# Performance work log

Hardware: AMD Instinct MI355X
Metric: run time of the kernel (lower is better)

Reference implementation:

```python
import jax, jax.numpy as jnp
import numpy as np

NS, NV = 48, 10            # scalar / vector multiplicities
IN_SIZE = NS + 3*NV + 3*NV + NS   # 156
N_EDGE_FEAT = 96
HIDDEN = 96
# weight shapes per output irrep: 0e:(58,48) 1o:(68,10) 1e:(68,10) 0o:(58,48)
W_SHAPES = [('0e', NS + NV, NS), ('1o', NS + 2*NV, NV), ('1e', 2*NV + NS, NV), ('0o', NV + NS, NS)]
WEIGHT_NUMEL = sum(a*b for _, a, b in W_SHAPES)  # 6928
N_NODES, N_EDGES = 10000, 50000


def setup_inputs() -> dict:
    key = jax.random.key(0)
    ks = jax.random.split(key, 9)
    node_attr = jax.random.normal(ks[0], (N_NODES, IN_SIZE), dtype=jnp.float32)
    edge_index = jax.random.randint(ks[1], (2, N_EDGES), 0, N_NODES)
    edge_attr = jax.random.normal(ks[2], (N_EDGES, N_EDGE_FEAT), dtype=jnp.float32)
    edge_sh = jax.random.normal(ks[3], (N_EDGES, 4), dtype=jnp.float32)
    s1 = 1.0 / np.sqrt(N_EDGE_FEAT)
    s2 = 1.0 / np.sqrt(HIDDEN)
    W1 = jax.random.normal(ks[4], (N_EDGE_FEAT, HIDDEN), dtype=jnp.float32) * s1
    b1 = jnp.zeros((HIDDEN,), dtype=jnp.float32)
    W2 = jax.random.normal(ks[5], (HIDDEN, WEIGHT_NUMEL), dtype=jnp.float32) * s2
    b2 = jnp.zeros((WEIGHT_NUMEL,), dtype=jnp.float32)
    return {'node_attr': node_attr, 'edge_index': edge_index, 'edge_attr': edge_attr,
            'edge_sh': edge_sh, 'W1': W1, 'b1': b1, 'W2': W2, 'b2': b2}


def _faster_tp(in_, sh, weight):
    # in_: [E, 156], sh: [E, 4], weight: [E, 6928]
    in_0e = in_[:, :NS]                                   # [E,48]
    in_1o = in_[:, NS:NS + 3*NV].reshape(-1, NV, 3)       # [E,10,3]
    in_1e = in_[:, NS + 3*NV:NS + 6*NV].reshape(-1, NV, 3)
    in_0o = in_[:, NS + 6*NV:]                            # [E,48]
    sh_0e = sh[:, 0]                                      # [E]
    sh_1o = sh[:, 1:]                                     # [E,3]
    inv_s3 = 1.0 / np.sqrt(3.0)
    inv_s2 = 1.0 / np.sqrt(2.0)

    out_0e = jnp.concatenate([
        in_0e * sh_0e[:, None],
        jnp.sum(in_1o * sh_1o[:, None, :], axis=-1) * inv_s3], axis=-1)      # [E,58]
    out_1o = jnp.concatenate([
        in_0e[:, :, None] * sh_1o[:, None, :],
        in_1o * sh_0e[:, None, None],
        jnp.cross(in_1e, sh_1o[:, None, :]) * inv_s2], axis=-2)              # [E,68,3]
    out_1e = jnp.concatenate([
        jnp.cross(in_1o, sh_1o[:, None, :]) * inv_s2,
        in_1e * sh_0e[:, None, None],
        in_0o[:, :, None] * sh_1o[:, None, :]], axis=-2)                     # [E,68,3]
    out_0o = jnp.concatenate([
        jnp.sum(in_1e * sh_1o[:, None, :], axis=-1) * inv_s3,
        in_0o * sh_0e[:, None]], axis=-1)                                    # [E,58]

    wd = {}
    start = 0
    for name, a, b in W_SHAPES:
        wd[name] = weight[:, start:start + a*b].reshape(-1, a, b) / np.sqrt(a)
        start += a*b

    o0e = jnp.einsum('ei,eio->eo', out_0e, wd['0e'])                 # [E,48]
    o1o = jnp.einsum('eic,eio->eoc', out_1o, wd['1o']).reshape(-1, 3*NV)
    o1e = jnp.einsum('eic,eio->eoc', out_1e, wd['1e']).reshape(-1, 3*NV)
    o0o = jnp.einsum('ei,eio->eo', out_0o, wd['0o'])                 # [E,48]
    return jnp.concatenate([o0e, o1o, o1e, o0o], axis=-1)           # [E,156]


def reference(node_attr, edge_index, edge_attr, edge_sh, W1, b1, W2, b2):
    edge_src, edge_dst = edge_index[0], edge_index[1]
    # edge MLP -> per-edge TP weights
    h = jax.nn.relu(edge_attr @ W1 + b1)
    w = h @ W2 + b2                                       # [E, 6928]
    tp = _faster_tp(node_attr[edge_dst], edge_sh, w)      # [E, 156]
    # scatter-mean over source nodes
    n = node_attr.shape[0]
    seg = jax.ops.segment_sum(tp, edge_src, num_segments=n)
    cnt = jax.ops.segment_sum(jnp.ones((tp.shape[0],), tp.dtype), edge_src, num_segments=n)
    out = seg / jnp.maximum(cnt, 1.0)[:, None]
    # residual (in/out sizes equal, so pad is a no-op)
    return out + node_attr
```

## Files before the change

### kernel.cpp

```cpp
#include <hip/hip_runtime.h>

#define NE 50000
#define NN 10000
#define KH 96
#define WN 6928
#define NTILE 484
#define IN_SZ 156
#define EPW 32

typedef __attribute__((ext_vector_type(8))) short short8;
typedef __attribute__((ext_vector_type(4))) float float4v;

template<int N> struct IC { static constexpr int n = N; };

__device__ __forceinline__ unsigned short f2bf(float x) {
  unsigned u = __float_as_uint(x);
  unsigned r = (u + 0x7FFFu + ((u >> 16) & 1u)) >> 16;
  return (unsigned short)r;
}
__device__ __forceinline__ float b2f(unsigned short u) {
  return __uint_as_float(((unsigned)u) << 16);
}

__device__ __forceinline__ void issue3(short8 (&B)[3], float &bv,
                                       const unsigned short* p, const float* pb) {
  asm volatile("global_load_dwordx4 %0, %4, off\n\t"
               "global_load_dwordx4 %1, %4, off offset:1024\n\t"
               "global_load_dwordx4 %2, %4, off offset:2048\n\t"
               "global_load_dword %3, %5, off"
               : "=&v"(B[0]), "=&v"(B[1]), "=&v"(B[2]), "=&v"(bv)
               : "v"(p), "v"(pb));
}
__device__ __forceinline__ void waitB8(short8 (&B)[3], float &bv) {
  asm volatile("s_waitcnt vmcnt(8)"
               : "+v"(B[0]), "+v"(B[1]), "+v"(B[2]), "+v"(bv));
}
__device__ __forceinline__ void waitB4(short8 (&B)[3], float &bv) {
  asm volatile("s_waitcnt vmcnt(4)"
               : "+v"(B[0]), "+v"(B[1]), "+v"(B[2]), "+v"(bv));
}
__device__ __forceinline__ void waitB0(short8 (&B)[3], float &bv) {
  asm volatile("s_waitcnt vmcnt(0)"
               : "+v"(B[0]), "+v"(B[1]), "+v"(B[2]), "+v"(bv));
}

__device__ __forceinline__ int col_of_np(int np) {
  if (np < 2784) return np;
  if (np < 3872) { int rel = np - 2784, i = rel >> 4, o = rel & 15; return (o < 10) ? 2784 + i * 10 + o : -1; }
  if (np < 4960) { int rel = np - 3872, i = rel >> 4, o = rel & 15; return (o < 10) ? 3464 + i * 10 + o : -1; }
  return 4144 + (np - 4960);
}

#define R0 (NTILE * 192)
#define R1 (R0 + NTILE * 16)
#define R2 (R1 + KH * KH)
#define R3 (R2 + NN * IN_SZ / 4)
#define R4 (R3 + NN / 4)
#define R5 (R4 + 192)
__global__ __launch_bounds__(256) void prep_kernel(
    const float* __restrict__ W2, const float* __restrict__ b2,
    const float* __restrict__ W1,
    unsigned short* __restrict__ W2PT, float* __restrict__ b2PT,
    unsigned short* __restrict__ W1T,
    float* __restrict__ acc, int* __restrict__ icnt,
    unsigned short* __restrict__ h_ext)
{
  int gid = blockIdx.x * 256 + threadIdx.x;
  if (gid < R0) {
    int lane = gid & 63, s = (gid >> 6) % 3, t = gid / 192;
    int l = lane & 15, q = lane >> 4;
    int c = col_of_np(t * 16 + l);
    int kbase = s * 32 + q * 8;
    unsigned short o8[8];
    #pragma unroll
    for (int j = 0; j < 8; ++j) {
      int k = kbase + j;
      float v = (c >= 0) ? W2[(size_t)k * WN + c] : 0.f;
      o8[j] = f2bf(v);
    }
    uint4 pk;
    pk.x = o8[0] | ((unsigned)o8[1] << 16);
    pk.y = o8[2] | ((unsigned)o8[3] << 16);
    pk.z = o8[4] | ((unsigned)o8[5] << 16);
    pk.w = o8[6] | ((unsigned)o8[7] << 16);
    *(uint4*)(W2PT + (size_t)gid * 8) = pk;
  } else if (gid < R1) {
    int j = gid - R0;
    int c = col_of_np(j);
    b2PT[j] = (c >= 0) ? b2[c] : 0.f;
  } else if (gid < R2) {
    int j = gid - R1;
    int c = j / KH, k = j - c * KH;
    W1T[c * KH + k] = f2bf(W1[k * KH + c]);
  } else if (gid < R3) {
    uint4 z = {0, 0, 0, 0};
    ((uint4*)acc)[gid - R2] = z;
  } else if (gid < R4) {
    uint4 z = {0, 0, 0, 0};
    ((uint4*)icnt)[gid - R3] = z;
  } else if (gid < R5) {
    uint4 z = {0, 0, 0, 0};
    ((uint4*)(h_ext + (size_t)NE * KH))[gid - R4] = z;
  }
}

__global__ __launch_bounds__(384) void mlp1_kernel(
    const float* __restrict__ edge_attr, const unsigned short* __restrict__ W1T,
    const float* __restrict__ b1, unsigned short* __restrict__ h_ext)
{
  const int tid = threadIdx.x;
  const int e0 = blockIdx.x * 16;
  const int w = tid >> 6, l = tid & 15, q = (tid >> 4) & 3;

  short8 a[3], b[3];
  #pragma unroll
  for (int s = 0; s < 3; ++s) {
    const float* pa = edge_attr + (size_t)(e0 + l) * KH + s * 32 + q * 8;
    float4 x = *(const float4*)pa, y = *(const float4*)(pa + 4);
    short8 t;
    t[0] = (short)f2bf(x.x); t[1] = (short)f2bf(x.y);
    t[2] = (short)f2bf(x.z); t[3] = (short)f2bf(x.w);
    t[4] = (short)f2bf(y.x); t[5] = (short)f2bf(y.y);
    t[6] = (short)f2bf(y.z); t[7] = (short)f2bf(y.w);
    a[s] = t;
    b[s] = *(const short8*)(W1T + (size_t)(w * 16 + l) * KH + s * 32 + q * 8);
  }
  float4v C = {0.f, 0.f, 0.f, 0.f};
  #pragma unroll
  for (int s = 0; s < 3; ++s)
    C = __builtin_amdgcn_mfma_f32_16x16x32_bf16(a[s], b[s], C, 0, 0, 0);

  float bv = b1[w * 16 + l];
  #pragma unroll
  for (int r = 0; r < 4; ++r)
    h_ext[(size_t)(e0 + q * 4 + r) * KH + w * 16 + l] = f2bf(fmaxf(C[r] + bv, 0.f));
}

__global__ __launch_bounds__(512, 4) void tp_kernel(
    const unsigned short* __restrict__ h_ext, const float* __restrict__ node_attr,
    const int* __restrict__ edge_index, const float* __restrict__ edge_sh,
    const unsigned short* __restrict__ W2PT, const float* __restrict__ b2PT,
    float* __restrict__ acc, int* __restrict__ icnt)
{
  __shared__ float sOut[EPW][IN_SZ];
  __shared__ unsigned short sF0[2][58][EPW];
  __shared__ unsigned short sF1[2][68][3][EPW];
  __shared__ float sShs[EPW][4];
  __shared__ int sSrc[EPW], sDst[EPW];

  const int tid = threadIdx.x;
  const int e0 = blockIdx.x * EPW;

  if (tid < EPW) {
    int ok = (e0 + tid) < NE;
    int s = ok ? edge_index[e0 + tid] : 0;
    int d = ok ? edge_index[NE + e0 + tid] : 0;
    sSrc[tid] = s; sDst[tid] = d;
    if (ok) atomicAdd(&icnt[s], 1);
  }
  if (tid >= 128 && tid < 256) {
    int t2 = tid - 128;
    int e = t2 >> 2, c = t2 & 3;
    sShs[e][c] = ((e0 + e) < NE) ? edge_sh[(size_t)(e0 + e) * 4 + c] : 0.f;
  }
  __syncthreads();

  {
    const int e = tid >> 4, j = tid & 15;
    const float* na = node_attr + (size_t)sDst[e] * IN_SZ;
    const float sh0 = sShs[e][0], sx = sShs[e][1], sy = sShs[e][2], sz = sShs[e][3];
    const float i3 = 0.57735026918962576f, i2 = 0.70710678118654752f;
    for (int i = j; i < 48; i += 16) {
      float v0 = na[i], w0 = na[108 + i];
      sF0[0][i][e] = f2bf(v0 * sh0);
      sF0[1][10 + i][e] = f2bf(w0 * sh0);
      sF1[0][i][0][e] = f2bf(v0 * sx); sF1[0][i][1][e] = f2bf(v0 * sy); sF1[0][i][2][e] = f2bf(v0 * sz);
      sF1[1][20 + i][0][e] = f2bf(w0 * sx); sF1[1][20 + i][1][e] = f2bf(w0 * sy); sF1[1][20 + i][2][e] = f2bf(w0 * sz);
    }
    if (j < 10) {
      const int v = j;
      float ax = na[48 + 3 * v], ay = na[48 + 3 * v + 1], az = na[48 + 3 * v + 2];
      float bx = na[78 + 3 * v], by = na[78 + 3 * v + 1], bz = na[78 + 3 * v + 2];
      sF0[0][48 + v][e] = f2bf((ax * sx + ay * sy + az * sz) * i3);
      sF0[1][v][e]      = f2bf((bx * sx + by * sy + bz * sz) * i3);
      sF1[0][48 + v][0][e] = f2bf(ax * sh0); sF1[0][48 + v][1][e] = f2bf(ay * sh0); sF1[0][48 + v][2][e] = f2bf(az * sh0);
      sF1[0][58 + v][0][e] = f2bf((by * sz - bz * sy) * i2);
      sF1[0][58 + v][1][e] = f2bf((bz * sx - bx * sz) * i2);
      sF1[0][58 + v][2][e] = f2bf((bx * sy - by * sx) * i2);
      sF1[1][v][0][e] = f2bf((ay * sz - az * sy) * i2);
      sF1[1][v][1][e] = f2bf((az * sx - ax * sz) * i2);
      sF1[1][v][2][e] = f2bf((ax * sy - ay * sx) * i2);
      sF1[1][10 + v][0][e] = f2bf(bx * sh0); sF1[1][10 + v][1][e] = f2bf(by * sh0); sF1[1][10 + v][2][e] = f2bf(bz * sh0);
    }
  }
  for (int idx = tid; idx < EPW * IN_SZ; idx += 512) (&sOut[0][0])[idx] = 0.f;
  __syncthreads();

  const int wv = tid >> 6, l = tid & 15, q = (tid >> 4) & 3;

  short8 Af[2][3];
  #pragma unroll
  for (int m = 0; m < 2; ++m) {
    const unsigned short* ar = h_ext + (size_t)(e0 + m * 16 + l) * KH + q * 8;
    #pragma unroll
    for (int s = 0; s < 3; ++s) Af[m][s] = *(const short8*)(ar + s * 32);
  }

  const unsigned short* wlane = W2PT + (size_t)(tid & 63) * 8;
  const float* blane = b2PT + l;

  auto sbody = [&](float (&a0)[4], float (&a1)[4], const short8 (&B)[3], float bv,
                   int sf, int i) {
    ushort4 f0 = *(const ushort4*)&sF0[sf][i][q * 4];
    ushort4 f1 = *(const ushort4*)&sF0[sf][i][16 + q * 4];
    float4v C0 = {bv, bv, bv, bv}, C1 = {bv, bv, bv, bv};
    #pragma unroll
    for (int s2 = 0; s2 < 3; ++s2) {
      C0 = __builtin_amdgcn_mfma_f32_16x16x32_bf16(Af[0][s2], B[s2], C0, 0, 0, 0);
      C1 = __builtin_amdgcn_mfma_f32_16x16x32_bf16(Af[1][s2], B[s2], C1, 0, 0, 0);
    }
    a0[0] += C0[0] * b2f(f0.x); a0[1] += C0[1] * b2f(f0.y);
    a0[2] += C0[2] * b2f(f0.z); a0[3] += C0[3] * b2f(f0.w);
    a1[0] += C1[0] * b2f(f1.x); a1[1] += C1[1] * b2f(f1.y);
    a1[2] += C1[2] * b2f(f1.z); a1[3] += C1[3] * b2f(f1.w);
  };
  auto sflush = [&](float (&a0)[4], float (&a1)[4], int col) {
    #pragma unroll
    for (int r = 0; r < 4; ++r) {
      unsafeAtomicAdd(&sOut[q * 4 + r][col],      a0[r]);
      unsafeAtomicAdd(&sOut[16 + q * 4 + r][col], a1[r]);
    }
  };

  auto run_scalar3 = [&](int sf, int ibeg, int tb, int obase, auto cnt) {
    constexpr int NSTEP = decltype(cnt)::n;
    #pragma unroll 1
    for (int ob = 0; ob < 3; ++ob) {
      float a0[4] = {0.f, 0.f, 0.f, 0.f}, a1[4] = {0.f, 0.f, 0.f, 0.f};
      short8 Ba[3], Bb[3], Bc[3];
      float vA, vB, vC;
      auto tadr = [&](int ii) -> size_t { return (size_t)(tb + 3 * (ibeg + ii) + ob); };
      { size_t t = tadr(0); issue3(Ba, vA, wlane + t * 1536, blane + t * 16); }
      { size_t t = tadr(1); issue3(Bb, vB, wlane + t * 1536, blane + t * 16); }
      { size_t t = tadr(2); issue3(Bc, vC, wlane + t * 1536, blane + t * 16); }
      #pragma unroll 1
      for (int ii = 0; ii < NSTEP - 3; ii += 3) {
        waitB8(Ba, vA); sbody(a0, a1, Ba, vA, sf, ibeg + ii);
        { size_t t = tadr(ii + 3); issue3(Ba, vA, wlane + t * 1536, blane + t * 16); }
        waitB8(Bb, vB); sbody(a0, a1, Bb, vB, sf, ibeg + ii + 1);
        { size_t t = tadr(ii + 4); issue3(Bb, vB, wlane + t * 1536, blane + t * 16); }
        waitB8(Bc, vC); sbody(a0, a1, Bc, vC, sf, ibeg + ii + 2);
        { size_t t = tadr(ii + 5); issue3(Bc, vC, wlane + t * 1536, blane + t * 16); }
      }
      waitB8(Ba, vA); sbody(a0, a1, Ba, vA, sf, ibeg + NSTEP - 3);
      waitB4(Bb, vB); sbody(a0, a1, Bb, vB, sf, ibeg + NSTEP - 2);
      waitB0(Bc, vC); sbody(a0, a1, Bc, vC, sf, ibeg + NSTEP - 1);
      sflush(a0, a1, obase + ob * 16 + l);
    }
  };

  auto run_scalar2 = [&](int sf, int ibeg, int tb, int obase, auto cnt) {
    constexpr int NSTEP = decltype(cnt)::n;
    #pragma unroll 1
    for (int ob = 0; ob < 3; ++ob) {
      float a0[4] = {0.f, 0.f, 0.f, 0.f}, a1[4] = {0.f, 0.f, 0.f, 0.f};
      short8 Ba[3], Bb[3];
      float vA, vB;
      auto tadr = [&](int ii) -> size_t { return (size_t)(tb + 3 * (ibeg + ii) + ob); };
      { size_t t = tadr(0); issue3(Ba, vA, wlane + t * 1536, blane + t * 16); }
      { size_t t = tadr(1); issue3(Bb, vB, wlane + t * 1536, blane + t * 16); }
      #pragma unroll 1
      for (int ii = 0; ii < NSTEP - 2; ii += 2) {
        waitB4(Ba, vA); sbody(a0, a1, Ba, vA, sf, ibeg + ii);
        { size_t t = tadr(ii + 2); issue3(Ba, vA, wlane + t * 1536, blane + t * 16); }
        waitB4(Bb, vB); sbody(a0, a1, Bb, vB, sf, ibeg + ii + 1);
        { size_t t = tadr(ii + 3); issue3(Bb, vB, wlane + t * 1536, blane + t * 16); }
      }
      waitB4(Ba, vA); sbody(a0, a1, Ba, vA, sf, ibeg + NSTEP - 2);
      waitB0(Bb, vB); sbody(a0, a1, Bb, vB, sf, ibeg + NSTEP - 1);
      sflush(a0, a1, obase + ob * 16 + l);
    }
  };

  if (wv < 4) {
    const int sf = wv >> 1;
    run_scalar3(sf, (wv & 1) * 21, sf ? 310 : 0, sf ? 108 : 0, IC<21>{});
  } else {
    const int vf = (wv >> 1) - 2;
    const int ibeg = (wv & 1) * 34;
    const int tb = vf ? 242 : 174;
    float r0[4][3] = {{0.f}}, r1[4][3] = {{0.f}};
    short8 Ba[3], Bb[3];
    float vA, vB;
    auto tadr = [&](int ii) -> size_t { return (size_t)(tb + ibeg + ii); };
    auto vbody = [&](const short8 (&B)[3], float bv, int ii) {
      int i = ibeg + ii;
      ushort4 g0[3], g1[3];
      #pragma unroll
      for (int cc = 0; cc < 3; ++cc) {
        g0[cc] = *(const ushort4*)&sF1[vf][i][cc][q * 4];
        g1[cc] = *(const ushort4*)&sF1[vf][i][cc][16 + q * 4];
      }
      float4v C0 = {bv, bv, bv, bv}, C1 = {bv, bv, bv, bv};
      #pragma unroll
      for (int s = 0; s < 3; ++s) {
        C0 = __builtin_amdgcn_mfma_f32_16x16x32_bf16(Af[0][s], B[s], C0, 0, 0, 0);
        C1 = __builtin_amdgcn_mfma_f32_16x16x32_bf16(Af[1][s], B[s], C1, 0, 0, 0);
      }
      #pragma unroll
      for (int cc = 0; cc < 3; ++cc) {
        r0[0][cc] += C0[0] * b2f(g0[cc].x); r0[1][cc] += C0[1] * b2f(g0[cc].y);
        r0[2][cc] += C0[2] * b2f(g0[cc].z); r0[3][cc] += C0[3] * b2f(g0[cc].w);
        r1[0][cc] += C1[0] * b2f(g1[cc].x); r1[1][cc] += C1[1] * b2f(g1[cc].y);
        r1[2][cc] += C1[2] * b2f(g1[cc].z); r1[3][cc] += C1[3] * b2f(g1[cc].w);
      }
    };
    { size_t t = tadr(0); issue3(Ba, vA, wlane + t * 1536, blane + t * 16); }
    { size_t t = tadr(1); issue3(Bb, vB, wlane + t * 1536, blane + t * 16); }
    #pragma unroll 1
    for (int ii = 0; ii < 32; ii += 2) {
      waitB4(Ba, vA); vbody(Ba, vA, ii);
      { size_t t = tadr(ii + 2); issue3(Ba, vA, wlane + t * 1536, blane + t * 16); }
      waitB4(Bb, vB); vbody(Bb, vB, ii + 1);
      { size_t t = tadr(ii + 3); issue3(Bb, vB, wlane + t * 1536, blane + t * 16); }
    }
    waitB4(Ba, vA); vbody(Ba, vA, 32);
    waitB0(Bb, vB); vbody(Bb, vB, 33);
    if (l < 10) {
      const int col = (vf ? 78 : 48) + 3 * l;
      #pragma unroll
      for (int r = 0; r < 4; ++r)
        #pragma unroll
        for (int cc = 0; cc < 3; ++cc) {
          unsafeAtomicAdd(&sOut[q * 4 + r][col + cc], r0[r][cc]);
          unsafeAtomicAdd(&sOut[16 + q * 4 + r][col + cc], r1[r][cc]);
        }
    }
    run_scalar2(vf, 42 + (wv & 1) * 8, vf ? 310 : 0, vf ? 108 : 0, IC<8>{});
  }
  __syncthreads();

  const float n58 = 0.13130643285972254f, n68 = 0.12126781251816650f;
  for (int idx = tid; idx < EPW * IN_SZ; idx += 512) {
    int e = idx / IN_SZ, o = idx - e * IN_SZ;
    if (e0 + e < NE) {
      float nrm = (o < 48 || o >= 108) ? n58 : n68;
      unsafeAtomicAdd(&acc[(size_t)sSrc[e] * IN_SZ + o], sOut[e][o] * nrm);
    }
  }
}

__global__ __launch_bounds__(256) void finalize_kernel(
    const float* __restrict__ acc, const int* __restrict__ icnt,
    const float* __restrict__ node_attr, float* __restrict__ out)
{
  int idx = blockIdx.x * 256 + threadIdx.x;
  if (idx < NN * IN_SZ) {
    int n = idx / IN_SZ;
    out[idx] = acc[idx] / fmaxf((float)icnt[n], 1.f) + node_attr[idx];
  }
}

extern "C" void kernel_launch(void* const* d_in, const int* in_sizes, int n_in,
                              void* d_out, int out_size, void* d_ws, size_t ws_size,
                              hipStream_t stream)
{
  const float* node_attr  = (const float*)d_in[0];
  const int*   edge_index = (const int*)d_in[1];
  const float* edge_attr  = (const float*)d_in[2];
  const float* edge_sh    = (const float*)d_in[3];
  const float* W1 = (const float*)d_in[4];
  const float* b1 = (const float*)d_in[5];
  const float* W2 = (const float*)d_in[6];
  const float* b2 = (const float*)d_in[7];
  float* out = (float*)d_out;

  unsigned short* h_ext = (unsigned short*)d_ws;
  unsigned short* W2PT  = h_ext + (size_t)50016 * KH;
  float* b2PT = (float*)(W2PT + (size_t)NTILE * 1536);
  float* acc  = b2PT + (size_t)NTILE * 16;
  int*   icnt = (int*)(acc + (size_t)NN * IN_SZ);
  unsigned short* W1T = (unsigned short*)(icnt + NN);

  prep_kernel<<<(R5 + 255) / 256, 256, 0, stream>>>(W2, b2, W1, W2PT, b2PT, W1T,
                                                    acc, icnt, h_ext);
  mlp1_kernel<<<NE / 16, 384, 0, stream>>>(edge_attr, W1T, b1, h_ext);
  tp_kernel<<<(NE + EPW - 1) / EPW, 512, 0, stream>>>(h_ext, node_attr, edge_index,
                                                      edge_sh, W2PT, b2PT, acc, icnt);
  finalize_kernel<<<(NN * IN_SZ + 255) / 256, 256, 0, stream>>>(acc, icnt, node_attr, out);
}
```

Before: 329.0 us.

## Process 64 edges per block to reuse streamed W2 tiles, rebalance wave work

Doubles the edges handled per tp_kernel block from 32 to 64. Each streamed W2 tile now feeds four 16-row MFMA groups instead of two, which roughly halves global W2 traffic per edge. The scalar-path split is reworked so that four waves each cover 30 padded input rows, with zeroed pad rows. Vector waves no longer take a scalar tail. Gathered node attributes are staged once into shared memory as bf16, which adds rounding on the inputs. The trade-offs are higher register and LDS use, launch bounds lowered to 2 blocks per CU, and some imbalance between the scalar and vector waves.

New measurement: 351.3 us. +6.8%, slower.

```diff
diff --git a/kernel.cpp b/kernel.cpp
--- a/kernel.cpp
+++ b/kernel.cpp
@@ -6,12 +6,10 @@
 #define WN 6928
 #define NTILE 484
 #define IN_SZ 156
-#define EPW 32
+#define EPW 64
 
 typedef __attribute__((ext_vector_type(8))) short short8;
 typedef __attribute__((ext_vector_type(4))) float float4v;
-
-template<int N> struct IC { static constexpr int n = N; };
 
 __device__ __forceinline__ unsigned short f2bf(float x) {
   unsigned u = __float_as_uint(x);
@@ -56,7 +54,7 @@
 #define R2 (R1 + KH * KH)
 #define R3 (R2 + NN * IN_SZ / 4)
 #define R4 (R3 + NN / 4)
-#define R5 (R4 + 192)
+#define R5 (R4 + 576)
 __global__ __launch_bounds__(256) void prep_kernel(
     const float* __restrict__ W2, const float* __restrict__ b2,
     const float* __restrict__ W1,
@@ -136,14 +134,15 @@
     h_ext[(size_t)(e0 + q * 4 + r) * KH + w * 16 + l] = f2bf(fmaxf(C[r] + bv, 0.f));
 }
 
-__global__ __launch_bounds__(512, 4) void tp_kernel(
+__global__ __launch_bounds__(512, 2) void tp_kernel(
     const unsigned short* __restrict__ h_ext, const float* __restrict__ node_attr,
     const int* __restrict__ edge_index, const float* __restrict__ edge_sh,
     const unsigned short* __restrict__ W2PT, const float* __restrict__ b2PT,
     float* __restrict__ acc, int* __restrict__ icnt)
 {
+  __shared__ unsigned short sIn[EPW][160];
   __shared__ float sOut[EPW][IN_SZ];
-  __shared__ unsigned short sF0[2][58][EPW];
+  __shared__ unsigned short sF0[2][60][EPW];
   __shared__ unsigned short sF1[2][68][3][EPW];
   __shared__ float sShs[EPW][4];
   __shared__ int sSrc[EPW], sDst[EPW];
@@ -158,29 +157,34 @@
     sSrc[tid] = s; sDst[tid] = d;
     if (ok) atomicAdd(&icnt[s], 1);
   }
-  if (tid >= 128 && tid < 256) {
+  if (tid >= 128 && tid < 384) {
     int t2 = tid - 128;
     int e = t2 >> 2, c = t2 & 3;
     sShs[e][c] = ((e0 + e) < NE) ? edge_sh[(size_t)(e0 + e) * 4 + c] : 0.f;
   }
   __syncthreads();
 
+  for (int idx = tid; idx < EPW * IN_SZ; idx += 512) {
+    int e = idx / IN_SZ, f = idx - e * IN_SZ;
+    sIn[e][f] = f2bf(node_attr[(size_t)sDst[e] * IN_SZ + f]);
+  }
+  for (int idx = tid; idx < EPW * IN_SZ; idx += 512) (&sOut[0][0])[idx] = 0.f;
+  __syncthreads();
+
   {
-    const int e = tid >> 4, j = tid & 15;
-    const float* na = node_attr + (size_t)sDst[e] * IN_SZ;
+    const int e = tid >> 3, j = tid & 7;
     const float sh0 = sShs[e][0], sx = sShs[e][1], sy = sShs[e][2], sz = sShs[e][3];
     const float i3 = 0.57735026918962576f, i2 = 0.70710678118654752f;
-    for (int i = j; i < 48; i += 16) {
-      float v0 = na[i], w0 = na[108 + i];
+    for (int i = j; i < 48; i += 8) {
+      float v0 = b2f(sIn[e][i]), w0 = b2f(sIn[e][108 + i]);
       sF0[0][i][e] = f2bf(v0 * sh0);
       sF0[1][10 + i][e] = f2bf(w0 * sh0);
       sF1[0][i][0][e] = f2bf(v0 * sx); sF1[0][i][1][e] = f2bf(v0 * sy); sF1[0][i][2][e] = f2bf(v0 * sz);
       sF1[1][20 + i][0][e] = f2bf(w0 * sx); sF1[1][20 + i][1][e] = f2bf(w0 * sy); sF1[1][20 + i][2][e] = f2bf(w0 * sz);
     }
-    if (j < 10) {
-      const int v = j;
-      float ax = na[48 + 3 * v], ay = na[48 + 3 * v + 1], az = na[48 + 3 * v + 2];
-      float bx = na[78 + 3 * v], by = na[78 + 3 * v + 1], bz = na[78 + 3 * v + 2];
+    for (int v = j; v < 10; v += 8) {
+      float ax = b2f(sIn[e][48 + 3 * v]), ay = b2f(sIn[e][48 + 3 * v + 1]), az = b2f(sIn[e][48 + 3 * v + 2]);
+      float bx = b2f(sIn[e][78 + 3 * v]), by = b2f(sIn[e][78 + 3 * v + 1]), bz = b2f(sIn[e][78 + 3 * v + 2]);
       sF0[0][48 + v][e] = f2bf((ax * sx + ay * sy + az * sz) * i3);
       sF0[1][v][e]      = f2bf((bx * sx + by * sy + bz * sz) * i3);
       sF1[0][48 + v][0][e] = f2bf(ax * sh0); sF1[0][48 + v][1][e] = f2bf(ay * sh0); sF1[0][48 + v][2][e] = f2bf(az * sh0);
@@ -193,14 +197,17 @@
       sF1[1][10 + v][0][e] = f2bf(bx * sh0); sF1[1][10 + v][1][e] = f2bf(by * sh0); sF1[1][10 + v][2][e] = f2bf(bz * sh0);
     }
   }
-  for (int idx = tid; idx < EPW * IN_SZ; idx += 512) (&sOut[0][0])[idx] = 0.f;
+  if (tid < 256) {
+    int fam = tid >> 7, i = 58 + ((tid >> 6) & 1), e = tid & 63;
+    sF0[fam][i][e] = 0;
+  }
   __syncthreads();
 
   const int wv = tid >> 6, l = tid & 15, q = (tid >> 4) & 3;
 
-  short8 Af[2][3];
+  short8 Af[4][3];
   #pragma unroll
-  for (int m = 0; m < 2; ++m) {
+  for (int m = 0; m < 4; ++m) {
     const unsigned short* ar = h_ext + (size_t)(e0 + m * 16 + l) * KH + q * 8;
     #pragma unroll
     for (int s = 0; s < 3; ++s) Af[m][s] = *(const short8*)(ar + s * 32);
@@ -209,103 +216,93 @@
   const unsigned short* wlane = W2PT + (size_t)(tid & 63) * 8;
   const float* blane = b2PT + l;
 
-  auto sbody = [&](float (&a0)[4], float (&a1)[4], const short8 (&B)[3], float bv,
+  auto sbody = [&](float (&a)[4][4], const short8 (&B)[3], float bv,
                    int sf, int i) {
     ushort4 f0 = *(const ushort4*)&sF0[sf][i][q * 4];
     ushort4 f1 = *(const ushort4*)&sF0[sf][i][16 + q * 4];
-    float4v C0 = {bv, bv, bv, bv}, C1 = {bv, bv, bv, bv};
+    ushort4 f2 = *(const ushort4*)&sF0[sf][i][32 + q * 4];
+    ushort4 f3 = *(const ushort4*)&sF0[sf][i][48 + q * 4];
+    float4v C0 = {bv, bv, bv, bv}, C1 = C0, C2 = C0, C3 = C0;
     #pragma unroll
     for (int s2 = 0; s2 < 3; ++s2) {
       C0 = __builtin_amdgcn_mfma_f32_16x16x32_bf16(Af[0][s2], B[s2], C0, 0, 0, 0);
       C1 = __builtin_amdgcn_mfma_f32_16x16x32_bf16(Af[1][s2], B[s2], C1, 0, 0, 0);
-    }
-    a0[0] += C0[0] * b2f(f0.x); a0[1] += C0[1] * b2f(f0.y);
-    a0[2] += C0[2] * b2f(f0.z); a0[3] += C0[3] * b2f(f0.w);
-    a1[0] += C1[0] * b2f(f1.x); a1[1] += C1[1] * b2f(f1.y);
-    a1[2] += C1[2] * b2f(f1.z); a1[3] += C1[3] * b2f(f1.w);
+      C2 = __builtin_amdgcn_mfma_f32_16x16x32_bf16(Af[2][s2], B[s2], C2, 0, 0, 0);
+      C3 = __builtin_amdgcn_mfma_f32_16x16x32_bf16(Af[3][s2], B[s2], C3, 0, 0, 0);
+    }
+    a[0][0] += C0[0] * b2f(f0.x); a[0][1] += C0[1] * b2f(f0.y);
+    a[0][2] += C0[2] * b2f(f0.z); a[0][3] += C0[3] * b2f(f0.w);
+    a[1][0] += C1[0] * b2f(f1.x); a[1][1] += C1[1] * b2f(f1.y);
+    a[1][2] += C1[2] * b2f(f1.z); a[1][3] += C1[3] * b2f(f1.w);
+    a[2][0] += C2[0] * b2f(f2.x); a[2][1] += C2[1] * b2f(f2.y);
+    a[2][2] += C2[2] * b2f(f2.z); a[2][3] += C2[3] * b2f(f2.w);
+    a[3][0] += C3[0] * b2f(f3.x); a[3][1] += C3[1] * b2f(f3.y);
+    a[3][2] += C3[2] * b2f(f3.z); a[3][3] += C3[3] * b2f(f3.w);
   };
-  auto sflush = [&](float (&a0)[4], float (&a1)[4], int col) {
+  auto sflush = [&](float (&a)[4][4], int col) {
     #pragma unroll
-    for (int r = 0; r < 4; ++r) {
-      unsafeAtomicAdd(&sOut[q * 4 + r][col],      a0[r]);
-      unsafeAtomicAdd(&sOut[16 + q * 4 + r][col], a1[r]);
-    }
+    for (int h = 0; h < 4; ++h)
+      #pragma unroll
+      for (int r = 0; r < 4; ++r)
+        unsafeAtomicAdd(&sOut[h * 16 + q * 4 + r][col], a[h][r]);
   };
 
-  auto run_scalar3 = [&](int sf, int ibeg, int tb, int obase, auto cnt) {
-    constexpr int NSTEP = decltype(cnt)::n;
+  if (wv < 4) {
+    const int sf = wv >> 1;
+    const int ibeg = (wv & 1) * 30;
+    const int tb = sf ? 310 : 0;
+    const int obase = sf ? 108 : 0;
     #pragma unroll 1
     for (int ob = 0; ob < 3; ++ob) {
-      float a0[4] = {0.f, 0.f, 0.f, 0.f}, a1[4] = {0.f, 0.f, 0.f, 0.f};
+      float a[4][4] = {{0.f,0.f,0.f,0.f},{0.f,0.f,0.f,0.f},{0.f,0.f,0.f,0.f},{0.f,0.f,0.f,0.f}};
       short8 Ba[3], Bb[3], Bc[3];
       float vA, vB, vC;
-      auto tadr = [&](int ii) -> size_t { return (size_t)(tb + 3 * (ibeg + ii) + ob); };
+      auto tadr = [&](int ii) -> size_t {
+        int i = ibeg + ii; if (i >= 58) i = ibeg;
+        return (size_t)(tb + 3 * i + ob);
+      };
       { size_t t = tadr(0); issue3(Ba, vA, wlane + t * 1536, blane + t * 16); }
       { size_t t = tadr(1); issue3(Bb, vB, wlane + t * 1536, blane + t * 16); }
       { size_t t = tadr(2); issue3(Bc, vC, wlane + t * 1536, blane + t * 16); }
       #pragma unroll 1
-      for (int ii = 0; ii < NSTEP - 3; ii += 3) {
-        waitB8(Ba, vA); sbody(a0, a1, Ba, vA, sf, ibeg + ii);
+      for (int ii = 0; ii < 27; ii += 3) {
+        waitB8(Ba, vA); sbody(a, Ba, vA, sf, ibeg + ii);
         { size_t t = tadr(ii + 3); issue3(Ba, vA, wlane + t * 1536, blane + t * 16); }
-        waitB8(Bb, vB); sbody(a0, a1, Bb, vB, sf, ibeg + ii + 1);
+        waitB8(Bb, vB); sbody(a, Bb, vB, sf, ibeg + ii + 1);
         { size_t t = tadr(ii + 4); issue3(Bb, vB, wlane + t * 1536, blane + t * 16); }
-        waitB8(Bc, vC); sbody(a0, a1, Bc, vC, sf, ibeg + ii + 2);
+        waitB8(Bc, vC); sbody(a, Bc, vC, sf, ibeg + ii + 2);
         { size_t t = tadr(ii + 5); issue3(Bc, vC, wlane + t * 1536, blane + t * 16); }
       }
-      waitB8(Ba, vA); sbody(a0, a1, Ba, vA, sf, ibeg + NSTEP - 3);
-      waitB4(Bb, vB); sbody(a0, a1, Bb, vB, sf, ibeg + NSTEP - 2);
-      waitB0(Bc, vC); sbody(a0, a1, Bc, vC, sf, ibeg + NSTEP - 1);
-      sflush(a0, a1, obase + ob * 16 + l);
-    }
-  };
-
-  auto run_scalar2 = [&](int sf, int ibeg, int tb, int obase, auto cnt) {
-    constexpr int NSTEP = decltype(cnt)::n;
-    #pragma unroll 1
-    for (int ob = 0; ob < 3; ++ob) {
-      float a0[4] = {0.f, 0.f, 0.f, 0.f}, a1[4] = {0.f, 0.f, 0.f, 0.f};
-      short8 Ba[3], Bb[3];
-      float vA, vB;
-      auto tadr = [&](int ii) -> size_t { return (size_t)(tb + 3 * (ibeg + ii) + ob); };
-      { size_t t = tadr(0); issue3(Ba, vA, wlane + t * 1536, blane + t * 16); }
-      { size_t t = tadr(1); issue3(Bb, vB, wlane + t * 1536, blane + t * 16); }
-      #pragma unroll 1
-      for (int ii = 0; ii < NSTEP - 2; ii += 2) {
-        waitB4(Ba, vA); sbody(a0, a1, Ba, vA, sf, ibeg + ii);
-        { size_t t = tadr(ii + 2); issue3(Ba, vA, wlane + t * 1536, blane + t * 16); }
-        waitB4(Bb, vB); sbody(a0, a1, Bb, vB, sf, ibeg + ii + 1);
-        { size_t t = tadr(ii + 3); issue3(Bb, vB, wlane + t * 1536, blane + t * 16); }
-      }
-      waitB4(Ba, vA); sbody(a0, a1, Ba, vA, sf, ibeg + NSTEP - 2);
-      waitB0(Bb, vB); sbody(a0, a1, Bb, vB, sf, ibeg + NSTEP - 1);
-      sflush(a0, a1, obase + ob * 16 + l);
-    }
-  };
-
-  if (wv < 4) {
-    const int sf = wv >> 1;
-    run_scalar3(sf, (wv & 1) * 21, sf ? 310 : 0, sf ? 108 : 0, IC<21>{});
+      waitB8(Ba, vA); sbody(a, Ba, vA, sf, ibeg + 27);
+      waitB4(Bb, vB); sbody(a, Bb, vB, sf, ibeg + 28);
+      waitB0(Bc, vC); sbody(a, Bc, vC, sf, ibeg + 29);
+      sflush(a, obase + ob * 16 + l);
+    }
   } else {
     const int vf = (wv >> 1) - 2;
     const int ibeg = (wv & 1) * 34;
     const int tb = vf ? 242 : 174;
-    float r0[4][3] = {{0.f}}, r1[4][3] = {{0.f}};
+    float r0[4][3] = {{0.f}}, r1[4][3] = {{0.f}}, r2[4][3] = {{0.f}}, r3[4][3] = {{0.f}};
     short8 Ba[3], Bb[3];
     float vA, vB;
     auto tadr = [&](int ii) -> size_t { return (size_t)(tb + ibeg + ii); };
     auto vbody = [&](const short8 (&B)[3], float bv, int ii) {
       int i = ibeg + ii;
-      ushort4 g0[3], g1[3];
+      ushort4 g0[3], g1[3], g2[3], g3[3];
       #pragma unroll
       for (int cc = 0; cc < 3; ++cc) {
         g0[cc] = *(const ushort4*)&sF1[vf][i][cc][q * 4];
         g1[cc] = *(const ushort4*)&sF1[vf][i][cc][16 + q * 4];
+        g2[cc] = *(const ushort4*)&sF1[vf][i][cc][32 + q * 4];
+        g3[cc] = *(const ushort4*)&sF1[vf][i][cc][48 + q * 4];
       }
-      float4v C0 = {bv, bv, bv, bv}, C1 = {bv, bv, bv, bv};
+      float4v C0 = {bv, bv, bv, bv}, C1 = C0, C2 = C0, C3 = C0;
       #pragma unroll
       for (int s = 0; s < 3; ++s) {
         C0 = __builtin_amdgcn_mfma_f32_16x16x32_bf16(Af[0][s], B[s], C0, 0, 0, 0);
         C1 = __builtin_amdgcn_mfma_f32_16x16x32_bf16(Af[1][s], B[s], C1, 0, 0, 0);
+        C2 = __builtin_amdgcn_mfma_f32_16x16x32_bf16(Af[2][s], B[s], C2, 0, 0, 0);
+        C3 = __builtin_amdgcn_mfma_f32_16x16x32_bf16(Af[3][s], B[s], C3, 0, 0, 0);
       }
       #pragma unroll
       for (int cc = 0; cc < 3; ++cc) {
@@ -313,6 +310,10 @@
         r0[2][cc] += C0[2] * b2f(g0[cc].z); r0[3][cc] += C0[3] * b2f(g0[cc].w);
         r1[0][cc] += C1[0] * b2f(g1[cc].x); r1[1][cc] += C1[1] * b2f(g1[cc].y);
         r1[2][cc] += C1[2] * b2f(g1[cc].z); r1[3][cc] += C1[3] * b2f(g1[cc].w);
+        r2[0][cc] += C2[0] * b2f(g2[cc].x); r2[1][cc] += C2[1] * b2f(g2[cc].y);
+        r2[2][cc] += C2[2] * b2f(g2[cc].z); r2[3][cc] += C2[3] * b2f(g2[cc].w);
+        r3[0][cc] += C3[0] * b2f(g3[cc].x); r3[1][cc] += C3[1] * b2f(g3[cc].y);
+        r3[2][cc] += C3[2] * b2f(g3[cc].z); r3[3][cc] += C3[3] * b2f(g3[cc].w);
       }
     };
     { size_t t = tadr(0); issue3(Ba, vA, wlane + t * 1536, blane + t * 16); }
@@ -332,11 +333,12 @@
       for (int r = 0; r < 4; ++r)
         #pragma unroll
         for (int cc = 0; cc < 3; ++cc) {
-          unsafeAtomicAdd(&sOut[q * 4 + r][col + cc], r0[r][cc]);
+          unsafeAtomicAdd(&sOut[q * 4 + r][col + cc],      r0[r][cc]);
           unsafeAtomicAdd(&sOut[16 + q * 4 + r][col + cc], r1[r][cc]);
+          unsafeAtomicAdd(&sOut[32 + q * 4 + r][col + cc], r2[r][cc]);
+          unsafeAtomicAdd(&sOut[48 + q * 4 + r][col + cc], r3[r][cc]);
         }
     }
-    run_scalar2(vf, 42 + (wv & 1) * 8, vf ? 310 : 0, vf ? 108 : 0, IC<8>{});
   }
   __syncthreads();
 
@@ -376,7 +378,7 @@
   float* out = (float*)d_out;
 
   unsigned short* h_ext = (unsigned short*)d_ws;
-  unsigned short* W2PT  = h_ext + (size_t)50016 * KH;
+  unsigned short* W2PT  = h_ext + (size_t)50048 * KH;
   float* b2PT = (float*)(W2PT + (size_t)NTILE * 1536);
   float* acc  = b2PT + (size_t)NTILE * 16;
   int*   icnt = (int*)(acc + (size_t)NN * IN_SZ);
```
